# Kernel optimization log

Hardware: AMD Instinct MI355X
Metric: run time of the kernel (lower is better)

## Reference

```python
import jax, jax.numpy as jnp
import numpy as np

N = 65536
H = 1024
E = 3  # experts: SwishGLU, GEGLU, ReGLU


def setup_inputs() -> dict:
    key = jax.random.key(0)
    ks = jax.random.split(key, 10)
    s = 1.0 / np.sqrt(H)
    return {
        "x": jax.random.normal(ks[0], (N, H), jnp.float32),
        "W1": jax.random.normal(ks[1], (E, H, H), jnp.float32) * s,
        "b1": jax.random.normal(ks[2], (E, H), jnp.float32) * s,
        "W2": jax.random.normal(ks[3], (E, H, H), jnp.float32) * s,
        "b2": jax.random.normal(ks[4], (E, H), jnp.float32) * s,
        "W3": jax.random.normal(ks[5], (E, H, H), jnp.float32) * s,
        "b3": jax.random.normal(ks[6], (E, H), jnp.float32) * s,
        "Wg": jax.random.normal(ks[7], (H, E), jnp.float32) * s,
        "bg": jax.random.normal(ks[8], (E,), jnp.float32) * s,
        "gumbel_u": jax.random.uniform(ks[9], (N, E), jnp.float32),
    }


def reference(x, W1, b1, W2, b2, W3, b3, Wg, bg, gumbel_u):
    # Gate: hard gumbel-softmax (tau=1, hard=True) with straight-through estimator
    logits = x @ Wg + bg                                   # [N, E]
    u = jnp.clip(gumbel_u, 1e-6, 1.0 - 1e-6)
    g = -jnp.log(-jnp.log(u))                              # Gumbel(0,1) noise
    y_soft = jax.nn.softmax(logits + g, axis=-1)           # [N, E]
    y_hard = jax.nn.one_hot(jnp.argmax(y_soft, axis=-1), E, dtype=x.dtype)
    gate = y_hard + y_soft - jax.lax.stop_gradient(y_soft)  # values == y_hard

    # Dense compute of all three GLU experts (faithful to original module)
    h1 = jnp.einsum('nd,edh->enh', x, W1) + b1[:, None, :]  # [E, N, H]
    h3 = jnp.einsum('nd,edh->enh', x, W3) + b3[:, None, :]  # [E, N, H]
    acts = jnp.stack([
        jax.nn.silu(h1[0]),                       # SwishGLU
        jax.nn.gelu(h1[1], approximate=False),    # GEGLU (exact erf gelu)
        jax.nn.relu(h1[2]),                       # ReGLU
    ], axis=0)                                    # [E, N, H]
    inner = acts * h3                             # [E, N, H]
    out_e = jnp.einsum('end,edh->enh', inner, W2) + b2[:, None, :]  # [E, N, H]

    # Select/mix with (hard) gate weights
    return jnp.einsum('enh,ne->nh', out_e, gate)  # [N, H]
```

## Files before the change

### kernel.cpp

```cpp
#include <hip/hip_runtime.h>
#include <math.h>

#define N_TOK 65536
#define H_DIM 1024

typedef __attribute__((ext_vector_type(8))) short bf16x8;
typedef __attribute__((ext_vector_type(4))) float f32x4;

static const size_t WS_CNT   = 0;
static const size_t WS_OFFS  = 64;
static const size_t WS_PERM  = 128;
static const size_t WS_WT13  = 1ull << 20;
static const size_t WS_WT2   = WS_WT13 + 12582912ull;
static const size_t WS_XB    = 20ull << 20;
static const size_t WS_INNER = WS_XB + 134217728ull;

static __device__ __forceinline__ unsigned short f2bf(float f) {
  union { float f; unsigned int u; } v; v.f = f;
  unsigned int r = v.u + 0x7fffu + ((v.u >> 16) & 1u);
  return (unsigned short)(r >> 16);
}

static __device__ __forceinline__ float fast_exp2(float x) {
  float r; asm("v_exp_f32 %0, %1" : "=v"(r) : "v"(x)); return r;
}
static __device__ __forceinline__ float fast_rcp(float x) {
  float r; asm("v_rcp_f32 %0, %1" : "=v"(r) : "v"(x)); return r;
}

static __device__ __forceinline__ void gload16(const void* g, void* l) {
  __builtin_amdgcn_global_load_lds(
      (const __attribute__((address_space(1))) unsigned int*)g,
      (__attribute__((address_space(3))) unsigned int*)l, 16, 0, 0);
}

static __device__ __forceinline__ void bar() {
  asm volatile("" ::: "memory");
  __builtin_amdgcn_s_barrier();
  asm volatile("" ::: "memory");
}

__global__ void init_kernel(int* cnt) {
  if (threadIdx.x < 4) cnt[threadIdx.x] = 0;
}

__global__ __launch_bounds__(1024) void gate_kernel(
    const float* __restrict__ x, const float* __restrict__ Wg,
    const float* __restrict__ bg, const float* __restrict__ gu,
    unsigned short* __restrict__ xb, int* __restrict__ cnt,
    int* __restrict__ perm)
{
  __shared__ float wg[3072];
  __shared__ int bexp[16];
  for (int i = threadIdx.x; i < 3072; i += 1024)
    wg[(i % 3) * 1024 + (i / 3)] = Wg[i];
  __syncthreads();
  const int wave = threadIdx.x >> 6;
  const int lane = threadIdx.x & 63;
  const int n0 = blockIdx.x * 16;
  const int n = n0 + wave;
  const float4* xrow = (const float4*)(x + (size_t)n * H_DIM);
  unsigned short* xbrow = xb + (size_t)n * H_DIM;
  float s0 = 0.f, s1 = 0.f, s2 = 0.f;
#pragma unroll
  for (int j = 0; j < 4; j++) {
    float4 v = xrow[j * 64 + lane];
    int d0 = (j * 64 + lane) * 4;
    float4 a0 = *(const float4*)&wg[d0];
    float4 a1 = *(const float4*)&wg[1024 + d0];
    float4 a2 = *(const float4*)&wg[2048 + d0];
    s0 += v.x * a0.x + v.y * a0.y + v.z * a0.z + v.w * a0.w;
    s1 += v.x * a1.x + v.y * a1.y + v.z * a1.z + v.w * a1.w;
    s2 += v.x * a2.x + v.y * a2.y + v.z * a2.z + v.w * a2.w;
    uint2 p;
    p.x = (unsigned)f2bf(v.x) | ((unsigned)f2bf(v.y) << 16);
    p.y = (unsigned)f2bf(v.z) | ((unsigned)f2bf(v.w) << 16);
    ((uint2*)xbrow)[j * 64 + lane] = p;
  }
#pragma unroll
  for (int o = 32; o; o >>= 1) {
    s0 += __shfl_xor(s0, o);
    s1 += __shfl_xor(s1, o);
    s2 += __shfl_xor(s2, o);
  }
  if (lane == 0) {
    const float* u = gu + (size_t)n * 3;
    float l[3] = { s0 + bg[0], s1 + bg[1], s2 + bg[2] };
    int best = 0; float bs = -1e30f;
#pragma unroll
    for (int e = 0; e < 3; e++) {
      float uc = fminf(fmaxf(u[e], 1e-6f), 1.f - 1e-6f);
      float g = -logf(-logf(uc));
      float s = l[e] + g;
      if (s > bs) { bs = s; best = e; }
    }
    bexp[wave] = best;
  }
  __syncthreads();
  if (threadIdx.x == 0) {
    int lc[3] = {0, 0, 0};
    int lpos[16];
    for (int w = 0; w < 16; w++) lpos[w] = lc[bexp[w]]++;
    int lbase[3];
    for (int e = 0; e < 3; e++)
      lbase[e] = lc[e] ? atomicAdd(&cnt[e], lc[e]) : 0;
    for (int w = 0; w < 16; w++) {
      int e = bexp[w];
      perm[e * N_TOK + lbase[e] + lpos[w]] = n0 + w;
    }
  }
}

__global__ void offs_kernel(const int* __restrict__ cnt, int* __restrict__ offs) {
  offs[0] = 0; offs[1] = cnt[0]; offs[2] = cnt[0] + cnt[1]; offs[3] = N_TOK;
}

__global__ __launch_bounds__(256) void wcvt_kernel(
    const float* __restrict__ W1, const float* __restrict__ W3,
    const float* __restrict__ W2,
    unsigned short* __restrict__ wt13, unsigned short* __restrict__ wt2)
{
  const int z = blockIdx.z, e = z / 3, m = z % 3;
  const float* src = (m == 0 ? W1 : (m == 1 ? W3 : W2)) + ((size_t)e << 20);
  __shared__ float t[64][33];
  const int h0 = blockIdx.x * 32, d0 = blockIdx.y * 64;
  const int tid = threadIdx.x;
  const int lh = tid & 31, lk = tid >> 5;
#pragma unroll
  for (int j = 0; j < 8; j++)
    t[j * 8 + lk][lh] = src[(size_t)(d0 + j * 8 + lk) * H_DIM + h0 + lh];
  __syncthreads();
  const int h_l = tid >> 3, kc = tid & 7;
  const int h = h0 + h_l;
  unsigned short sv[8];
#pragma unroll
  for (int j = 0; j < 8; j++) sv[j] = f2bf(t[kc * 8 + j][h_l]);
  const int kpos = d0 + ((kc ^ (h & 7)) << 3);
  if (m == 2) {
    *(uint4*)&wt2[((size_t)e << 20) + ((size_t)h << 10) + kpos] = *(const uint4*)sv;
  } else {
    const int nc = ((h >> 4) << 5) + (m << 4) + (h & 15);
    *(uint4*)&wt13[((size_t)e << 21) + ((size_t)nc << 10) + kpos] = *(const uint4*)sv;
  }
}

#define MFMA16(d, bb, aa) d = __builtin_amdgcn_mfma_f32_16x16x32_bf16((bb), (aa), (d), 0, 0, 0)

template<int PH>
__global__ __launch_bounds__(512, 2) void mlp_kernel(
    const unsigned short* __restrict__ A,
    const unsigned short* __restrict__ B,
    const float* __restrict__ bA, const float* __restrict__ bB,
    const int* __restrict__ cnt, const int* __restrict__ offs,
    const int* __restrict__ perm,
    unsigned short* __restrict__ inner, float* __restrict__ out)
{
  constexpr int NXT = (PH == 1) ? 8 : 4;
  const int e = blockIdx.z;
  const int ce = cnt[e];
  const int f = blockIdx.x + NXT * blockIdx.y;
  const int mt = (f & 7) + 8 * ((f >> 3) / NXT);
  const int nt = (f >> 3) % NXT;
  const int m0 = mt << 8;
  if (m0 >= ce) return;
  const int n0 = nt << 8;
  const int oe = offs[e];

  __shared__ short smem[65536];

  const int tid = threadIdx.x;
  const int wid = tid >> 6, lane = tid & 63;
  const int wm = (wid >> 2) * 128, wn = (wid & 3) * 64;
  const int lr = lane & 15, quad = lane >> 4;
  const int xa = lane & 7;
  const int sl = lane >> 3, sc = lane & 7;

  unsigned aoff[4], boff[4];
  int ldsA[4], ldsB[4];
#pragma unroll
  for (int h = 0; h < 2; h++)
#pragma unroll
    for (int si = 0; si < 2; si++) {
      const int hs = h * 2 + si;
      const int rowb = h * 128 + (wid + si * 8) * 8;
      const int r = rowb + sl;
      unsigned arow;
      if constexpr (PH == 1) {
        arow = (unsigned)perm[e * N_TOK + min(m0 + r, ce - 1)];
      } else {
        arow = (unsigned)(oe + min(m0 + r, ce - 1));
      }
      aoff[hs] = (arow << 10) + (unsigned)((sc ^ sl) << 3);
      const unsigned brow = (PH == 1 ? ((unsigned)e << 11) : ((unsigned)e << 10))
                          + (unsigned)(n0 + r);
      boff[hs] = (brow << 10) + (unsigned)(sc << 3);
      ldsA[hs] = rowb * 64;
      ldsB[hs] = 16384 + rowb * 64;
    }

  f32x4 acc[8][4];
#pragma unroll
  for (int i = 0; i < 8; i++)
#pragma unroll
    for (int j = 0; j < 4; j++) acc[i][j] = (f32x4){0.f, 0.f, 0.f, 0.f};

#define ISSA(d, hs, k0) gload16(A + aoff[hs] + (k0), &smem[(d) * 32768 + ldsA[hs]])
#define ISSB(d, hs, k0) gload16(B + boff[hs] + (k0), &smem[(d) * 32768 + ldsB[hs]])
#define LDA_(mi, kx) (*(const bf16x8*)&As[(wm + (mi) * 16 + lr) * 64 + (((((kx) << 2) + quad) ^ xa) << 3)])
#define LDB_(nj, kx) (*(const bf16x8*)&Bs[(wn + (nj) * 16 + lr) * 64 + (((((kx) << 2) + quad) ^ xa) << 3)])

  ISSA(0, 0, 0);  ISSA(0, 1, 0);  ISSA(0, 2, 0);  ISSA(0, 3, 0);
  ISSB(0, 0, 0);  ISSB(0, 1, 0);  ISSB(0, 2, 0);  ISSB(0, 3, 0);
  ISSB(1, 0, 64); ISSB(1, 1, 64); ISSB(1, 2, 64); ISSB(1, 3, 64);
  asm volatile("s_waitcnt vmcnt(4)" ::: "memory");
  bar();

#pragma unroll 2
  for (int tt = 0; tt < 16; tt++) {
    const int cur = tt & 1, nxt = cur ^ 1;
    const short* As = smem + cur * 32768;
    const short* Bs = As + 16384;
    const int k1 = (tt + 1) << 6, k2 = (tt + 2) << 6;
    bf16x8 af[8], bf0[4], ag[8], bg1[4];

#pragma unroll
    for (int mi = 0; mi < 8; mi++) af[mi] = LDA_(mi, 0);
#pragma unroll
    for (int nj = 0; nj < 4; nj++) bf0[nj] = LDB_(nj, 0);
    if (tt < 15) { ISSA(nxt, 0, k1); ISSA(nxt, 1, k1); ISSA(nxt, 2, k1); ISSA(nxt, 3, k1); }
    __builtin_amdgcn_s_setprio(1);
#pragma unroll
    for (int mi = 0; mi < 8; mi++)
#pragma unroll
      for (int nj = 0; nj < 4; nj++)
        MFMA16(acc[mi][nj], bf0[nj], af[mi]);
    __builtin_amdgcn_s_setprio(0);
#pragma unroll
    for (int mi = 0; mi < 8; mi++) ag[mi] = LDA_(mi, 1);
#pragma unroll
    for (int nj = 0; nj < 4; nj++) bg1[nj] = LDB_(nj, 1);
    __builtin_amdgcn_s_setprio(1);
#pragma unroll
    for (int mi = 0; mi < 8; mi++)
#pragma unroll
      for (int nj = 0; nj < 4; nj++)
        MFMA16(acc[mi][nj], bg1[nj], ag[mi]);
    __builtin_amdgcn_s_setprio(0);

    bar();
    if (tt < 14) { ISSB(cur, 0, k2); ISSB(cur, 1, k2); ISSB(cur, 2, k2); ISSB(cur, 3, k2); }
    if (tt < 14)      asm volatile("s_waitcnt vmcnt(4)" ::: "memory");
    else if (tt < 15) asm volatile("s_waitcnt vmcnt(0)" ::: "memory");
    if (tt < 15) bar();
  }

#undef ISSA
#undef ISSB
#undef LDA_
#undef LDB_

  if constexpr (PH == 1) {
    const int colg = (((n0 + wn) >> 5) << 4) + quad * 4;
#pragma unroll
    for (int p = 0; p < 2; p++) {
      const int colb = colg + p * 16;
      const float4 v1 = *(const float4*)&bA[e * H_DIM + colb];
      const float4 v3 = *(const float4*)&bB[e * H_DIM + colb];
#pragma unroll
      for (int mi = 0; mi < 8; mi++) {
        const int rr = m0 + wm + mi * 16 + lr;
        if (rr < ce) {
          unsigned short sv[4];
#pragma unroll
          for (int r = 0; r < 4; r++) {
            const float h1 = acc[mi][2 * p][r]     + ((const float*)&v1)[r];
            const float h3 = acc[mi][2 * p + 1][r] + ((const float*)&v3)[r];
            float a;
            if (e == 0)      a = h1 * fast_rcp(1.f + fast_exp2(h1 * -1.44269504f));
            else if (e == 1) a = 0.5f * h1 * (1.f + erff(h1 * 0.70710678118f));
            else             a = fmaxf(h1, 0.f);
            sv[r] = f2bf(a * h3);
          }
          *(uint2*)&inner[((size_t)(oe + rr) << 10) + colb] = *(const uint2*)sv;
        }
      }
    }
  } else {
#pragma unroll
    for (int nj = 0; nj < 4; nj++) {
      const int colb = n0 + wn + nj * 16 + quad * 4;
      const float4 v2 = *(const float4*)&bA[e * H_DIM + colb];
#pragma unroll
      for (int mi = 0; mi < 8; mi++) {
        const int rr = m0 + wm + mi * 16 + lr;
        if (rr < ce) {
          const int g = perm[e * N_TOK + rr];
          float4 v;
          v.x = acc[mi][nj][0] + v2.x;
          v.y = acc[mi][nj][1] + v2.y;
          v.z = acc[mi][nj][2] + v2.z;
          v.w = acc[mi][nj][3] + v2.w;
          *(float4*)&out[((size_t)g << 10) + colb] = v;
        }
      }
    }
  }
}

extern "C" void kernel_launch(void* const* d_in, const int* in_sizes, int n_in,
                              void* d_out, int out_size, void* d_ws, size_t ws_size,
                              hipStream_t stream)
{
  const float* x  = (const float*)d_in[0];
  const float* W1 = (const float*)d_in[1];
  const float* b1 = (const float*)d_in[2];
  const float* W2 = (const float*)d_in[3];
  const float* b2 = (const float*)d_in[4];
  const float* W3 = (const float*)d_in[5];
  const float* b3 = (const float*)d_in[6];
  const float* Wg = (const float*)d_in[7];
  const float* bg = (const float*)d_in[8];
  const float* gu = (const float*)d_in[9];
  float* out = (float*)d_out;

  char* ws = (char*)d_ws;
  int* cnt  = (int*)(ws + WS_CNT);
  int* offs = (int*)(ws + WS_OFFS);
  int* perm = (int*)(ws + WS_PERM);
  unsigned short* wt13 = (unsigned short*)(ws + WS_WT13);
  unsigned short* wt2  = (unsigned short*)(ws + WS_WT2);
  unsigned short* xb   = (unsigned short*)(ws + WS_XB);
  unsigned short* inner = (unsigned short*)(ws + WS_INNER);

  init_kernel<<<1, 64, 0, stream>>>(cnt);
  gate_kernel<<<N_TOK / 16, 1024, 0, stream>>>(x, Wg, bg, gu, xb, cnt, perm);
  offs_kernel<<<1, 1, 0, stream>>>(cnt, offs);
  wcvt_kernel<<<dim3(32, 16, 9), 256, 0, stream>>>(W1, W3, W2, wt13, wt2);
  mlp_kernel<1><<<dim3(8, 256, 3), 512, 0, stream>>>(
      xb, wt13, b1, b3, cnt, offs, perm, inner, nullptr);
  mlp_kernel<2><<<dim3(4, 256, 3), 512, 0, stream>>>(
      inner, wt2, b2, nullptr, cnt, offs, perm, nullptr, out);
}
```

Measured before the change: 1.070 ms.

## Load B fragments directly from global, halve LDS, batch gate rows per block

The GEMM kernels no longer stage the weight (B) tile through LDS. Each wave reads its B fragments straight from global memory, which is laid out unswizzled so the wcvt kernel drops its XOR swizzle. Shared memory per block is halved and one barrier and the B wait per k-step are removed. The trade is that every wave re-fetches B from global or L2 with higher latency and no cross-wave reuse. Separately, the gate kernel handles 64 tokens per block and builds the per-expert permutation with ballot/popcount instead of a serial single-thread loop.

```diff
diff --git a/kernel.cpp b/kernel.cpp
--- a/kernel.cpp
+++ b/kernel.cpp
@@ -51,63 +51,70 @@
     int* __restrict__ perm)
 {
   __shared__ float wg[3072];
-  __shared__ int bexp[16];
+  __shared__ int bexp[64];
   for (int i = threadIdx.x; i < 3072; i += 1024)
     wg[(i % 3) * 1024 + (i / 3)] = Wg[i];
   __syncthreads();
   const int wave = threadIdx.x >> 6;
   const int lane = threadIdx.x & 63;
-  const int n0 = blockIdx.x * 16;
-  const int n = n0 + wave;
-  const float4* xrow = (const float4*)(x + (size_t)n * H_DIM);
-  unsigned short* xbrow = xb + (size_t)n * H_DIM;
-  float s0 = 0.f, s1 = 0.f, s2 = 0.f;
-#pragma unroll
-  for (int j = 0; j < 4; j++) {
-    float4 v = xrow[j * 64 + lane];
-    int d0 = (j * 64 + lane) * 4;
-    float4 a0 = *(const float4*)&wg[d0];
-    float4 a1 = *(const float4*)&wg[1024 + d0];
-    float4 a2 = *(const float4*)&wg[2048 + d0];
-    s0 += v.x * a0.x + v.y * a0.y + v.z * a0.z + v.w * a0.w;
-    s1 += v.x * a1.x + v.y * a1.y + v.z * a1.z + v.w * a1.w;
-    s2 += v.x * a2.x + v.y * a2.y + v.z * a2.z + v.w * a2.w;
-    uint2 p;
-    p.x = (unsigned)f2bf(v.x) | ((unsigned)f2bf(v.y) << 16);
-    p.y = (unsigned)f2bf(v.z) | ((unsigned)f2bf(v.w) << 16);
-    ((uint2*)xbrow)[j * 64 + lane] = p;
-  }
-#pragma unroll
-  for (int o = 32; o; o >>= 1) {
-    s0 += __shfl_xor(s0, o);
-    s1 += __shfl_xor(s1, o);
-    s2 += __shfl_xor(s2, o);
-  }
-  if (lane == 0) {
-    const float* u = gu + (size_t)n * 3;
-    float l[3] = { s0 + bg[0], s1 + bg[1], s2 + bg[2] };
-    int best = 0; float bs = -1e30f;
-#pragma unroll
-    for (int e = 0; e < 3; e++) {
-      float uc = fminf(fmaxf(u[e], 1e-6f), 1.f - 1e-6f);
-      float g = -logf(-logf(uc));
-      float s = l[e] + g;
-      if (s > bs) { bs = s; best = e; }
-    }
-    bexp[wave] = best;
+  const int n0 = blockIdx.x * 64;
+#pragma unroll 1
+  for (int r = 0; r < 4; r++) {
+    const int n = n0 + wave * 4 + r;
+    const float4* xrow = (const float4*)(x + (size_t)n * H_DIM);
+    unsigned short* xbrow = xb + (size_t)n * H_DIM;
+    float s0 = 0.f, s1 = 0.f, s2 = 0.f;
+#pragma unroll
+    for (int j = 0; j < 4; j++) {
+      float4 v = xrow[j * 64 + lane];
+      int d0 = (j * 64 + lane) * 4;
+      float4 a0 = *(const float4*)&wg[d0];
+      float4 a1 = *(const float4*)&wg[1024 + d0];
+      float4 a2 = *(const float4*)&wg[2048 + d0];
+      s0 += v.x * a0.x + v.y * a0.y + v.z * a0.z + v.w * a0.w;
+      s1 += v.x * a1.x + v.y * a1.y + v.z * a1.z + v.w * a1.w;
+      s2 += v.x * a2.x + v.y * a2.y + v.z * a2.z + v.w * a2.w;
+      uint2 p;
+      p.x = (unsigned)f2bf(v.x) | ((unsigned)f2bf(v.y) << 16);
+      p.y = (unsigned)f2bf(v.z) | ((unsigned)f2bf(v.w) << 16);
+      ((uint2*)xbrow)[j * 64 + lane] = p;
+    }
+#pragma unroll
+    for (int o = 32; o; o >>= 1) {
+      s0 += __shfl_xor(s0, o);
+      s1 += __shfl_xor(s1, o);
+      s2 += __shfl_xor(s2, o);
+    }
+    if (lane == 0) {
+      const float* u = gu + (size_t)n * 3;
+      float l[3] = { s0 + bg[0], s1 + bg[1], s2 + bg[2] };
+      int best = 0; float bs = -1e30f;
+#pragma unroll
+      for (int e = 0; e < 3; e++) {
+        float uc = fminf(fmaxf(u[e], 1e-6f), 1.f - 1e-6f);
+        float g = -logf(-logf(uc));
+        float s = l[e] + g;
+        if (s > bs) { bs = s; best = e; }
+      }
+      bexp[wave * 4 + r] = best;
+    }
   }
   __syncthreads();
-  if (threadIdx.x == 0) {
-    int lc[3] = {0, 0, 0};
-    int lpos[16];
-    for (int w = 0; w < 16; w++) lpos[w] = lc[bexp[w]]++;
-    int lbase[3];
-    for (int e = 0; e < 3; e++)
-      lbase[e] = lc[e] ? atomicAdd(&cnt[e], lc[e]) : 0;
-    for (int w = 0; w < 16; w++) {
-      int e = bexp[w];
-      perm[e * N_TOK + lbase[e] + lpos[w]] = n0 + w;
-    }
+  if (wave == 0) {
+    const int mye = bexp[lane];
+    const unsigned long long m0 = __ballot(mye == 0);
+    const unsigned long long m1 = __ballot(mye == 1);
+    const unsigned long long m2 = __ballot(mye == 2);
+    int base = 0;
+    if (lane < 3) {
+      const unsigned long long mk = lane == 0 ? m0 : (lane == 1 ? m1 : m2);
+      base = atomicAdd(&cnt[lane], __popcll(mk));
+    }
+    const int b0 = __shfl(base, 0), b1 = __shfl(base, 1), b2 = __shfl(base, 2);
+    const unsigned long long mymask = mye == 0 ? m0 : (mye == 1 ? m1 : m2);
+    const int mybase = mye == 0 ? b0 : (mye == 1 ? b1 : b2);
+    const int pos = mybase + (int)__popcll(mymask & ((1ull << lane) - 1ull));
+    perm[mye * N_TOK + pos] = n0 + lane;
   }
 }
 
@@ -135,7 +142,7 @@
   unsigned short sv[8];
 #pragma unroll
   for (int j = 0; j < 8; j++) sv[j] = f2bf(t[kc * 8 + j][h_l]);
-  const int kpos = d0 + ((kc ^ (h & 7)) << 3);
+  const int kpos = d0 + (kc << 3);
   if (m == 2) {
     *(uint4*)&wt2[((size_t)e << 20) + ((size_t)h << 10) + kpos] = *(const uint4*)sv;
   } else {
@@ -147,7 +154,7 @@
 #define MFMA16(d, bb, aa) d = __builtin_amdgcn_mfma_f32_16x16x32_bf16((bb), (aa), (d), 0, 0, 0)
 
 template<int PH>
-__global__ __launch_bounds__(512, 2) void mlp_kernel(
+static __device__ __forceinline__ void mlp_core(
     const unsigned short* __restrict__ A,
     const unsigned short* __restrict__ B,
     const float* __restrict__ bA, const float* __restrict__ bB,
@@ -166,7 +173,7 @@
   const int n0 = nt << 8;
   const int oe = offs[e];
 
-  __shared__ short smem[65536];
+  __shared__ short smem[32768];
 
   const int tid = threadIdx.x;
   const int wid = tid >> 6, lane = tid & 63;
@@ -175,8 +182,8 @@
   const int xa = lane & 7;
   const int sl = lane >> 3, sc = lane & 7;
 
-  unsigned aoff[4], boff[4];
-  int ldsA[4], ldsB[4];
+  unsigned aoff[4];
+  int ldsA[4];
 #pragma unroll
   for (int h = 0; h < 2; h++)
 #pragma unroll
@@ -191,12 +198,11 @@
         arow = (unsigned)(oe + min(m0 + r, ce - 1));
       }
       aoff[hs] = (arow << 10) + (unsigned)((sc ^ sl) << 3);
-      const unsigned brow = (PH == 1 ? ((unsigned)e << 11) : ((unsigned)e << 10))
-                          + (unsigned)(n0 + r);
-      boff[hs] = (brow << 10) + (unsigned)(sc << 3);
       ldsA[hs] = rowb * 64;
-      ldsB[hs] = 16384 + rowb * 64;
-    }
+    }
+
+  const unsigned browE = (PH == 1 ? ((unsigned)e << 11) : ((unsigned)e << 10));
+  const unsigned short* bbase = B + ((size_t)(browE + n0 + wn + lr) << 10) + quad * 8;
 
   f32x4 acc[8][4];
 #pragma unroll
@@ -204,58 +210,54 @@
 #pragma unroll
     for (int j = 0; j < 4; j++) acc[i][j] = (f32x4){0.f, 0.f, 0.f, 0.f};
 
-#define ISSA(d, hs, k0) gload16(A + aoff[hs] + (k0), &smem[(d) * 32768 + ldsA[hs]])
-#define ISSB(d, hs, k0) gload16(B + boff[hs] + (k0), &smem[(d) * 32768 + ldsB[hs]])
+#define ISSA(d, hs, k0g) gload16(A + aoff[hs] + (k0g), &smem[(d) * 16384 + ldsA[hs]])
 #define LDA_(mi, kx) (*(const bf16x8*)&As[(wm + (mi) * 16 + lr) * 64 + (((((kx) << 2) + quad) ^ xa) << 3)])
-#define LDB_(nj, kx) (*(const bf16x8*)&Bs[(wn + (nj) * 16 + lr) * 64 + (((((kx) << 2) + quad) ^ xa) << 3)])
-
-  ISSA(0, 0, 0);  ISSA(0, 1, 0);  ISSA(0, 2, 0);  ISSA(0, 3, 0);
-  ISSB(0, 0, 0);  ISSB(0, 1, 0);  ISSB(0, 2, 0);  ISSB(0, 3, 0);
-  ISSB(1, 0, 64); ISSB(1, 1, 64); ISSB(1, 2, 64); ISSB(1, 3, 64);
-  asm volatile("s_waitcnt vmcnt(4)" ::: "memory");
+#define LDB_(nj, kx, k0g) (*(const bf16x8*)(bbase + (nj) * 16384 + (k0g) + ((kx) << 5)))
+
+  ISSA(0, 0, 0); ISSA(0, 1, 0); ISSA(0, 2, 0); ISSA(0, 3, 0);
+  asm volatile("s_waitcnt vmcnt(0)" ::: "memory");
   bar();
 
 #pragma unroll 2
   for (int tt = 0; tt < 16; tt++) {
     const int cur = tt & 1, nxt = cur ^ 1;
-    const short* As = smem + cur * 32768;
-    const short* Bs = As + 16384;
-    const int k1 = (tt + 1) << 6, k2 = (tt + 2) << 6;
-    bf16x8 af[8], bf0[4], ag[8], bg1[4];
-
-#pragma unroll
-    for (int mi = 0; mi < 8; mi++) af[mi] = LDA_(mi, 0);
-#pragma unroll
-    for (int nj = 0; nj < 4; nj++) bf0[nj] = LDB_(nj, 0);
+    const short* As = smem + cur * 16384;
+    const int k0 = tt << 6, k1 = (tt + 1) << 6;
+
     if (tt < 15) { ISSA(nxt, 0, k1); ISSA(nxt, 1, k1); ISSA(nxt, 2, k1); ISSA(nxt, 3, k1); }
+    asm volatile("" ::: "memory");
+
+    bf16x8 b[4][2];
+#pragma unroll
+    for (int nj = 0; nj < 4; nj++)
+#pragma unroll
+      for (int kx = 0; kx < 2; kx++)
+        b[nj][kx] = LDB_(nj, kx, k0);
+
+    bf16x8 a[8];
+#pragma unroll
+    for (int mi = 0; mi < 8; mi++) a[mi] = LDA_(mi, 0);
     __builtin_amdgcn_s_setprio(1);
 #pragma unroll
     for (int mi = 0; mi < 8; mi++)
 #pragma unroll
       for (int nj = 0; nj < 4; nj++)
-        MFMA16(acc[mi][nj], bf0[nj], af[mi]);
+        MFMA16(acc[mi][nj], b[nj][0], a[mi]);
     __builtin_amdgcn_s_setprio(0);
 #pragma unroll
-    for (int mi = 0; mi < 8; mi++) ag[mi] = LDA_(mi, 1);
-#pragma unroll
-    for (int nj = 0; nj < 4; nj++) bg1[nj] = LDB_(nj, 1);
+    for (int mi = 0; mi < 8; mi++) a[mi] = LDA_(mi, 1);
     __builtin_amdgcn_s_setprio(1);
 #pragma unroll
     for (int mi = 0; mi < 8; mi++)
 #pragma unroll
       for (int nj = 0; nj < 4; nj++)
-        MFMA16(acc[mi][nj], bg1[nj], ag[mi]);
+        MFMA16(acc[mi][nj], b[nj][1], a[mi]);
     __builtin_amdgcn_s_setprio(0);
 
-    bar();
-    if (tt < 14) { ISSB(cur, 0, k2); ISSB(cur, 1, k2); ISSB(cur, 2, k2); ISSB(cur, 3, k2); }
-    if (tt < 14)      asm volatile("s_waitcnt vmcnt(4)" ::: "memory");
-    else if (tt < 15) asm volatile("s_waitcnt vmcnt(0)" ::: "memory");
     if (tt < 15) bar();
   }
 
 #undef ISSA
-#undef ISSB
 #undef LDA_
 #undef LDB_
 
@@ -307,6 +309,24 @@
   }
 }
 
+__global__ __launch_bounds__(512, 2) void mlp1_kernel(
+    const unsigned short* __restrict__ A, const unsigned short* __restrict__ B,
+    const float* __restrict__ bA, const float* __restrict__ bB,
+    const int* __restrict__ cnt, const int* __restrict__ offs,
+    const int* __restrict__ perm, unsigned short* __restrict__ inner)
+{
+  mlp_core<1>(A, B, bA, bB, cnt, offs, perm, inner, nullptr);
+}
+
+__global__ __launch_bounds__(512, 2) void mlp2_kernel(
+    const unsigned short* __restrict__ A, const unsigned short* __restrict__ B,
+    const float* __restrict__ bA,
+    const int* __restrict__ cnt, const int* __restrict__ offs,
+    const int* __restrict__ perm, float* __restrict__ out)
+{
+  mlp_core<2>(A, B, bA, nullptr, cnt, offs, perm, nullptr, out);
+}
+
 extern "C" void kernel_launch(void* const* d_in, const int* in_sizes, int n_in,
                               void* d_out, int out_size, void* d_ws, size_t ws_size,
                               hipStream_t stream)
@@ -333,11 +353,11 @@
   unsigned short* inner = (unsigned short*)(ws + WS_INNER);
 
   init_kernel<<<1, 64, 0, stream>>>(cnt);
-  gate_kernel<<<N_TOK / 16, 1024, 0, stream>>>(x, Wg, bg, gu, xb, cnt, perm);
+  gate_kernel<<<N_TOK / 64, 1024, 0, stream>>>(x, Wg, bg, gu, xb, cnt, perm);
   offs_kernel<<<1, 1, 0, stream>>>(cnt, offs);
   wcvt_kernel<<<dim3(32, 16, 9), 256, 0, stream>>>(W1, W3, W2, wt13, wt2);
-  mlp_kernel<1><<<dim3(8, 256, 3), 512, 0, stream>>>(
-      xb, wt13, b1, b3, cnt, offs, perm, inner, nullptr);
-  mlp_kernel<2><<<dim3(4, 256, 3), 512, 0, stream>>>(
-      inner, wt2, b2, nullptr, cnt, offs, perm, nullptr, out);
-}
+  mlp1_kernel<<<dim3(8, 256, 3), 512, 0, stream>>>(
+      xb, wt13, b1, b3, cnt, offs, perm, inner);
+  mlp2_kernel<<<dim3(4, 256, 3), 512, 0, stream>>>(
+      inner, wt2, b2, cnt, offs, perm, out);
+}
```

Measured after the change: 1.330 ms. 24.2% more time.
